# Performance work log

Measured on AMD Instinct MI355X. Metric: run time of the kernel, lower is better.

## Reference

```python
import jax, jax.numpy as jnp
import numpy as np

DIM = 16
FDIM = 16
KNN = 10
N = 1_000_000


def setup_inputs() -> dict:
    key = jax.random.key(0)
    k1, k2, k3, k4, k5, k6 = jax.random.split(key, 6)
    xknn = jax.random.normal(k1, (N, DIM, KNN), dtype=jnp.float32)
    x = jax.random.normal(k2, (N, DIM), dtype=jnp.float32)
    # mlpF = Conv1d(dim, F, 1): weight [F, dim] (kernel size 1 squeezed), bias [F]
    s = 1.0 / np.sqrt(DIM)
    Wf = jax.random.normal(k3, (FDIM, DIM), dtype=jnp.float32) * s
    bf = jax.random.normal(k4, (FDIM,), dtype=jnp.float32) * s
    # mlp1 = Conv1d(F, 1, 1): weight [F], bias scalar
    s1 = 1.0 / np.sqrt(FDIM)
    W1 = jax.random.normal(k5, (FDIM,), dtype=jnp.float32) * s1
    b1 = jax.random.normal(k6, (), dtype=jnp.float32) * s1
    return {"xknn": xknn, "x": x, "Wf": Wf, "bf": bf, "W1": W1, "b1": b1}


def reference(xknn, x, Wf, bf, W1, b1):
    n = xknn.shape[0]
    x2 = xknn.reshape(n, DIM, KNN)                       # [N, dim, K]
    # mlpF on neighbors: Conv1d(dim->F, k=1)
    h2 = jnp.einsum('fd,ndk->nfk', Wf, x2) + bf[:, None]  # [N, F, K]
    a2 = jnp.einsum('f,nfk->nk', W1, h2)[:, None, :] + b1  # mlp1 -> [N, 1, K]
    # mlpF + mlp1 on center point
    x1 = x.reshape(n, DIM, 1)
    h1 = jnp.einsum('fd,ndk->nfk', Wf, x1) + bf[:, None]   # [N, F, 1]
    a1 = jnp.einsum('f,nfk->nk', W1, h1) + b1              # [N, 1] (squeeze+unsqueeze)
    # per-slice additive attention logits (the python loop in the original)
    logits = a2 + a1[:, :, None]                           # [N, 1, K]
    # torch Fn.softmax with implicit dim on 3D tensor -> dim=0 (faithful)
    xc = jax.nn.softmax(logits, axis=0)                    # [N, 1, K]
    # values: mlpF(x2) again, then a raw reshape [N,F,K]->[N,K,F] (not transpose)
    x2v = h2.reshape(n, KNN, FDIM)                         # [N, K, F]
    x_attn = jnp.matmul(xc, x2v)                           # [N, 1, F]
    return x_attn.squeeze(), x2v
```

## Files before the change

### kernel.cpp

```cpp
#include <hip/hip_runtime.h>
#include <math.h>


__device__ __forceinline__ void comb(float& m, float& s, float om, float os) {
  float M = fmaxf(m, om);
  if (M == -INFINITY) return;
  s = s * __expf(m - M) + os * __expf(om - M);
  m = M;
}

template <int CTRL>
__device__ __forceinline__ float dppmov(float v) {
  return __int_as_float(__builtin_amdgcn_update_dpp(
      0, __float_as_int(v), CTRL, 0xf, 0xf, true));
}

__device__ __forceinline__ float osum(float v) {
  v += dppmov<0xB1>(v);
  v += dppmov<0x4E>(v);
  v += dppmov<0x141>(v);
  return v;
}

__device__ __forceinline__ float f4e(const float4& v, int e) {
  return (e == 0) ? v.x : (e == 1) ? v.y : (e == 2) ? v.z : v.w;
}

__global__ __launch_bounds__(256) void gap_k1(
    const float* __restrict__ xknn, const float* __restrict__ x,
    const float* __restrict__ Wf, const float* __restrict__ bf,
    const float* __restrict__ W1, const float* __restrict__ b1p,
    float* __restrict__ out, float* __restrict__ partials, int n) {
  __shared__ float s_red[4][16][2];

  const int tid = threadIdx.x;
  const int o = tid & 7;
  const int c = o & 3;
  const int p8 = tid >> 3;
  const int lane = tid & 63;
  const int wave = tid >> 6;

  float wfo[2][16], w1o[2], bfo[2];
#pragma unroll
  for (int fp = 0; fp < 2; ++fp) {
    const float* wr = Wf + (size_t)(2 * o + fp) * 16;
#pragma unroll
    for (int dq = 0; dq < 4; ++dq) {
      float4 v = *(const float4*)(wr + dq * 4);
      wfo[fp][dq * 4 + 0] = v.x;
      wfo[fp][dq * 4 + 1] = v.y;
      wfo[fp][dq * 4 + 2] = v.z;
      wfo[fp][dq * 4 + 3] = v.w;
    }
    w1o[fp] = W1[2 * o + fp];
    bfo[fp] = bf[2 * o + fp];
  }
  const float b1v = b1p[0];

  float u2[2];
  {
    float ufull[16];
#pragma unroll
    for (int d = 0; d < 16; ++d)
      ufull[d] = fmaf(w1o[1], wfo[1][d], w1o[0] * wfo[0][d]);
#pragma unroll
    for (int mk = 1; mk < 8; mk <<= 1)
#pragma unroll
      for (int d = 0; d < 16; ++d) ufull[d] += __shfl_xor(ufull[d], mk);
#pragma unroll
    for (int j = 0; j < 2; ++j) {
      float v = ufull[j];
#pragma unroll
      for (int oo = 1; oo < 8; ++oo) v = (o == oo) ? ufull[2 * oo + j] : v;
      u2[j] = v;
    }
  }
  float sb = fmaf(w1o[1], bfo[1], w1o[0] * bfo[0]);
  sb += __shfl_xor(sb, 1);
  sb += __shfl_xor(sb, 2);
  sb += __shfl_xor(sb, 4);
  const float addA = sb + 2.0f * b1v;

  float rm[2] = {-INFINITY, -INFINITY}, rs[2] = {0.f, 0.f};

  float* out0 = out;
  float* out1 = out + (size_t)n * 16;

  const long pt0 = (long)blockIdx.x * 32 + p8;
  const long pstride = (long)gridDim.x * 32;

  for (long pt = pt0; pt < n; pt += pstride) {
    const float* rowq = xknn + (size_t)pt * 160 + 40 * c;
    float4 own[10];
#pragma unroll
    for (int j = 0; j < 10; ++j) own[j] = *(const float4*)(rowq + 4 * j);
    const float2 xc = *(const float2*)(x + (size_t)pt * 16 + 2 * o);

    float acc0[10], acc1[10];
#pragma unroll
    for (int k = 0; k < 10; ++k) {
      acc0[k] = bfo[0];
      acc1[k] = bfo[1];
    }
#pragma unroll
    for (int src = 0; src < 4; ++src) {
#pragma unroll
      for (int rr = 0; rr < 40; ++rr) {
        const int r = 40 * src + rr;
        const int d = r / 10, k = r - d * 10;
        const float mine = f4e(own[rr >> 2], rr & 3);
        const float xv = (src == 0)   ? dppmov<0x00>(mine)
                         : (src == 1) ? dppmov<0x55>(mine)
                         : (src == 2) ? dppmov<0xAA>(mine)
                                      : dppmov<0xFF>(mine);
        acc0[k] = fmaf(wfo[0][d], xv, acc0[k]);
        acc1[k] = fmaf(wfo[1][d], xv, acc1[k]);
      }
    }

    float* o1 = out1 + (size_t)pt * 160 + 20 * o;
    *(float4*)(o1 + 0) = make_float4(acc0[0], acc0[1], acc0[2], acc0[3]);
    *(float4*)(o1 + 4) = make_float4(acc0[4], acc0[5], acc0[6], acc0[7]);
    *(float4*)(o1 + 8) = make_float4(acc0[8], acc0[9], acc1[0], acc1[1]);
    *(float4*)(o1 + 12) = make_float4(acc1[2], acc1[3], acc1[4], acc1[5]);
    *(float4*)(o1 + 16) = make_float4(acc1[6], acc1[7], acc1[8], acc1[9]);

    float tk[10];
#pragma unroll
    for (int k = 0; k < 10; ++k)
      tk[k] = osum(fmaf(w1o[1], acc1[k], w1o[0] * acc0[k]));

    const float a1u = osum(fmaf(u2[1], xc.y, u2[0] * xc.x));
    const float addc = a1u + addA;

    float lj0 = 0.f, lj1 = 0.f;
#pragma unroll
    for (int kk = 0; kk < 10; ++kk) {
      lj0 = (kk == 2 * o) ? (tk[kk] + addc) : lj0;
      lj1 = (kk == 2 * o + 1) ? (tk[kk] + addc) : lj1;
    }

    *(float2*)(out0 + (size_t)pt * 16 + 2 * o) = make_float2(lj0, lj1);
    if (o < 5) {
      comb(rm[0], rs[0], lj0, 1.0f);
      comb(rm[1], rs[1], lj1, 1.0f);
    }
  }

#pragma unroll
  for (int mk = 8; mk < 64; mk <<= 1) {
#pragma unroll
    for (int j = 0; j < 2; ++j) {
      float om = __shfl_xor(rm[j], mk);
      float os = __shfl_xor(rs[j], mk);
      comb(rm[j], rs[j], om, os);
    }
  }
  if (lane < 5) {
#pragma unroll
    for (int j = 0; j < 2; ++j) {
      s_red[wave][2 * lane + j][0] = rm[j];
      s_red[wave][2 * lane + j][1] = rs[j];
    }
  }
  __syncthreads();
  if (tid < 10) {
    float m = s_red[0][tid][0], s = s_red[0][tid][1];
    comb(m, s, s_red[1][tid][0], s_red[1][tid][1]);
    comb(m, s, s_red[2][tid][0], s_red[2][tid][1]);
    comb(m, s, s_red[3][tid][0], s_red[3][tid][1]);
    partials[(size_t)blockIdx.x * 20 + tid * 2 + 0] = m;
    partials[(size_t)blockIdx.x * 20 + tid * 2 + 1] = s;
  }
}

__global__ __launch_bounds__(256) void gap_k2(const float* __restrict__ part,
                                              int nb, float* __restrict__ fin) {
  const int k = blockIdx.x;
  const int tid = threadIdx.x;
  float m = -INFINITY, s = 0.f;
  for (int i = tid; i < nb; i += 256)
    comb(m, s, part[(size_t)i * 20 + k * 2], part[(size_t)i * 20 + k * 2 + 1]);
#pragma unroll
  for (int mask = 1; mask < 64; mask <<= 1) {
    float om = __shfl_xor(m, mask, 64);
    float os = __shfl_xor(s, mask, 64);
    comb(m, s, om, os);
  }
  __shared__ float sm[4][2];
  const int wave = tid >> 6, lane = tid & 63;
  if (lane == 0) { sm[wave][0] = m; sm[wave][1] = s; }
  __syncthreads();
  if (tid == 0) {
    for (int w = 1; w < 4; ++w) comb(m, s, sm[w][0], sm[w][1]);
    fin[k * 2 + 0] = m;
    fin[k * 2 + 1] = s;
  }
}

__global__ __launch_bounds__(256) void gap_k3(const float* __restrict__ fin,
                                              float* __restrict__ out, int n) {
  __shared__ float s_fin[20];
  if (threadIdx.x < 20) s_fin[threadIdx.x] = fin[threadIdx.x];
  __syncthreads();
  float mk[10], rsk[10];
#pragma unroll
  for (int k = 0; k < 10; ++k) {
    mk[k] = s_fin[2 * k];
    rsk[k] = 1.0f / s_fin[2 * k + 1];
  }
  float* out0 = out;
  const float* out1 = out + (size_t)n * 16;
  const int q = threadIdx.x & 3;
  const int pl = threadIdx.x >> 2;
  for (long i = (long)blockIdx.x * 64 + pl; i < n; i += (long)gridDim.x * 64) {
    float* lrow = out0 + i * 16;
    float4 la = *(const float4*)(lrow);
    float4 lb = *(const float4*)(lrow + 4);
    float2 lc = *(const float2*)(lrow + 8);
    float l[10] = {la.x, la.y, la.z, la.w, lb.x, lb.y, lb.z, lb.w, lc.x, lc.y};
    float w[10];
#pragma unroll
    for (int k = 0; k < 10; ++k) w[k] = __expf(l[k] - mk[k]) * rsk[k];
    const float* vrow = out1 + i * 160 + q * 4;
    float4 acc = make_float4(0.f, 0.f, 0.f, 0.f);
#pragma unroll
    for (int k = 0; k < 10; ++k) {
      float4 v = *(const float4*)(vrow + k * 16);
      float wk = w[k];
      acc.x = fmaf(wk, v.x, acc.x);
      acc.y = fmaf(wk, v.y, acc.y);
      acc.z = fmaf(wk, v.z, acc.z);
      acc.w = fmaf(wk, v.w, acc.w);
    }
    *(float4*)(lrow + q * 4) = acc;
  }
}

extern "C" void kernel_launch(void* const* d_in, const int* in_sizes, int n_in,
                              void* d_out, int out_size, void* d_ws, size_t ws_size,
                              hipStream_t stream) {
  const float* xknn = (const float*)d_in[0];
  const float* x    = (const float*)d_in[1];
  const float* Wf   = (const float*)d_in[2];
  const float* bf   = (const float*)d_in[3];
  const float* W1   = (const float*)d_in[4];
  const float* b1   = (const float*)d_in[5];
  float* out = (float*)d_out;
  const int n = in_sizes[1] / 16;

  const int G1 = 2048;
  float* partials = (float*)d_ws;
  float* finals = partials + (size_t)G1 * 20;

  gap_k1<<<G1, 256, 0, stream>>>(xknn, x, Wf, bf, W1, b1, out, partials, n);
  gap_k2<<<10, 256, 0, stream>>>(partials, G1, finals);
  gap_k3<<<2048, 256, 0, stream>>>(finals, out, n);
}
```

Measured before the change: 559.7 us.

## Remap gap_k1 to 16 lanes per point with one feature per lane

Restructures the main kernel so each point is handled by 16 lanes, each owning one output feature and ten contiguous inputs, instead of 8 lanes owning two features each. Cross-lane broadcast of inputs now uses ds_swizzle within 16-lane groups rather than DPP quad broadcasts. The W1·Wf vector is precomputed per lane directly, and launch_bounds is dropped. This halves per-thread register use and FMAs per point, but swizzles go through the LDS crossbar and may be slower than DPP. Memory accesses shrink to float2 granularity.

```diff
diff --git a/kernel.cpp b/kernel.cpp
--- a/kernel.cpp
+++ b/kernel.cpp
@@ -9,159 +9,134 @@
   m = M;
 }
 
+template <int B>
+__device__ __forceinline__ float swz16(float v) {
+  return __int_as_float(
+      __builtin_amdgcn_ds_swizzle(__float_as_int(v), (B << 5) | 0x10));
+}
+
 template <int CTRL>
 __device__ __forceinline__ float dppmov(float v) {
   return __int_as_float(__builtin_amdgcn_update_dpp(
       0, __float_as_int(v), CTRL, 0xf, 0xf, true));
 }
 
-__device__ __forceinline__ float osum(float v) {
+__device__ __forceinline__ float sum16(float v) {
   v += dppmov<0xB1>(v);
   v += dppmov<0x4E>(v);
   v += dppmov<0x141>(v);
+  v += dppmov<0x140>(v);
   return v;
 }
 
-__device__ __forceinline__ float f4e(const float4& v, int e) {
-  return (e == 0) ? v.x : (e == 1) ? v.y : (e == 2) ? v.z : v.w;
-}
-
-__global__ __launch_bounds__(256) void gap_k1(
+__global__ void gap_k1(
     const float* __restrict__ xknn, const float* __restrict__ x,
     const float* __restrict__ Wf, const float* __restrict__ bf,
     const float* __restrict__ W1, const float* __restrict__ b1p,
     float* __restrict__ out, float* __restrict__ partials, int n) {
-  __shared__ float s_red[4][16][2];
+  __shared__ float s_red[4][10][2];
 
   const int tid = threadIdx.x;
-  const int o = tid & 7;
-  const int c = o & 3;
-  const int p8 = tid >> 3;
   const int lane = tid & 63;
   const int wave = tid >> 6;
-
-  float wfo[2][16], w1o[2], bfo[2];
-#pragma unroll
-  for (int fp = 0; fp < 2; ++fp) {
-    const float* wr = Wf + (size_t)(2 * o + fp) * 16;
-#pragma unroll
-    for (int dq = 0; dq < 4; ++dq) {
-      float4 v = *(const float4*)(wr + dq * 4);
-      wfo[fp][dq * 4 + 0] = v.x;
-      wfo[fp][dq * 4 + 1] = v.y;
-      wfo[fp][dq * 4 + 2] = v.z;
-      wfo[fp][dq * 4 + 3] = v.w;
-    }
-    w1o[fp] = W1[2 * o + fp];
-    bfo[fp] = bf[2 * o + fp];
-  }
-  const float b1v = b1p[0];
-
-  float u2[2];
-  {
-    float ufull[16];
-#pragma unroll
-    for (int d = 0; d < 16; ++d)
-      ufull[d] = fmaf(w1o[1], wfo[1][d], w1o[0] * wfo[0][d]);
-#pragma unroll
-    for (int mk = 1; mk < 8; mk <<= 1)
-#pragma unroll
-      for (int d = 0; d < 16; ++d) ufull[d] += __shfl_xor(ufull[d], mk);
-#pragma unroll
-    for (int j = 0; j < 2; ++j) {
-      float v = ufull[j];
-#pragma unroll
-      for (int oo = 1; oo < 8; ++oo) v = (o == oo) ? ufull[2 * oo + j] : v;
-      u2[j] = v;
-    }
-  }
-  float sb = fmaf(w1o[1], bfo[1], w1o[0] * bfo[0]);
-  sb += __shfl_xor(sb, 1);
-  sb += __shfl_xor(sb, 2);
-  sb += __shfl_xor(sb, 4);
-  const float addA = sb + 2.0f * b1v;
-
-  float rm[2] = {-INFINITY, -INFINITY}, rs[2] = {0.f, 0.f};
+  const int f = lane & 15;
+  const int pg = lane >> 4;
+
+  float wfo[16];
+#pragma unroll
+  for (int dq = 0; dq < 4; ++dq) {
+    float4 v = *(const float4*)(Wf + (size_t)f * 16 + 4 * dq);
+    wfo[4 * dq + 0] = v.x;
+    wfo[4 * dq + 1] = v.y;
+    wfo[4 * dq + 2] = v.z;
+    wfo[4 * dq + 3] = v.w;
+  }
+  const float w1o = W1[f];
+  const float bfo = bf[f];
+  float u_own = 0.f;
+#pragma unroll
+  for (int j = 0; j < 16; ++j) u_own = fmaf(W1[j], Wf[j * 16 + f], u_own);
+  const float addA = 2.0f * b1p[0];
+
+  float rm = -INFINITY, rs = 0.f;
 
   float* out0 = out;
   float* out1 = out + (size_t)n * 16;
 
-  const long pt0 = (long)blockIdx.x * 32 + p8;
-  const long pstride = (long)gridDim.x * 32;
+  const long pt0 = (long)blockIdx.x * 16 + wave * 4 + pg;
+  const long pstride = (long)gridDim.x * 16;
 
   for (long pt = pt0; pt < n; pt += pstride) {
-    const float* rowq = xknn + (size_t)pt * 160 + 40 * c;
-    float4 own[10];
-#pragma unroll
-    for (int j = 0; j < 10; ++j) own[j] = *(const float4*)(rowq + 4 * j);
-    const float2 xc = *(const float2*)(x + (size_t)pt * 16 + 2 * o);
-
-    float acc0[10], acc1[10];
-#pragma unroll
-    for (int k = 0; k < 10; ++k) {
-      acc0[k] = bfo[0];
-      acc1[k] = bfo[1];
-    }
-#pragma unroll
-    for (int src = 0; src < 4; ++src) {
-#pragma unroll
-      for (int rr = 0; rr < 40; ++rr) {
-        const int r = 40 * src + rr;
-        const int d = r / 10, k = r - d * 10;
-        const float mine = f4e(own[rr >> 2], rr & 3);
-        const float xv = (src == 0)   ? dppmov<0x00>(mine)
-                         : (src == 1) ? dppmov<0x55>(mine)
-                         : (src == 2) ? dppmov<0xAA>(mine)
-                                      : dppmov<0xFF>(mine);
-        acc0[k] = fmaf(wfo[0][d], xv, acc0[k]);
-        acc1[k] = fmaf(wfo[1][d], xv, acc1[k]);
+    const float* rowf = xknn + (size_t)pt * 160 + 10 * f;
+    float2 own[5];
+#pragma unroll
+    for (int j = 0; j < 5; ++j) own[j] = *(const float2*)(rowf + 2 * j);
+    const float xo = x[(size_t)pt * 16 + f];
+
+    float acc[10];
+#pragma unroll
+    for (int k = 0; k < 10; ++k) acc[k] = bfo;
+#pragma unroll
+    for (int d = 0; d < 16; ++d) {
+#pragma unroll
+      for (int j = 0; j < 10; ++j) {
+        const float mine = (j & 1) ? own[j >> 1].y : own[j >> 1].x;
+        float xv;
+        switch (d) {
+          case 0:  xv = swz16<0>(mine); break;
+          case 1:  xv = swz16<1>(mine); break;
+          case 2:  xv = swz16<2>(mine); break;
+          case 3:  xv = swz16<3>(mine); break;
+          case 4:  xv = swz16<4>(mine); break;
+          case 5:  xv = swz16<5>(mine); break;
+          case 6:  xv = swz16<6>(mine); break;
+          case 7:  xv = swz16<7>(mine); break;
+          case 8:  xv = swz16<8>(mine); break;
+          case 9:  xv = swz16<9>(mine); break;
+          case 10: xv = swz16<10>(mine); break;
+          case 11: xv = swz16<11>(mine); break;
+          case 12: xv = swz16<12>(mine); break;
+          case 13: xv = swz16<13>(mine); break;
+          case 14: xv = swz16<14>(mine); break;
+          default: xv = swz16<15>(mine); break;
+        }
+        acc[j] = fmaf(wfo[d], xv, acc[j]);
       }
     }
 
-    float* o1 = out1 + (size_t)pt * 160 + 20 * o;
-    *(float4*)(o1 + 0) = make_float4(acc0[0], acc0[1], acc0[2], acc0[3]);
-    *(float4*)(o1 + 4) = make_float4(acc0[4], acc0[5], acc0[6], acc0[7]);
-    *(float4*)(o1 + 8) = make_float4(acc0[8], acc0[9], acc1[0], acc1[1]);
-    *(float4*)(o1 + 12) = make_float4(acc1[2], acc1[3], acc1[4], acc1[5]);
-    *(float4*)(o1 + 16) = make_float4(acc1[6], acc1[7], acc1[8], acc1[9]);
+    float* o1 = out1 + (size_t)pt * 160 + 10 * f;
+    *(float2*)(o1 + 0) = make_float2(acc[0], acc[1]);
+    *(float2*)(o1 + 2) = make_float2(acc[2], acc[3]);
+    *(float2*)(o1 + 4) = make_float2(acc[4], acc[5]);
+    *(float2*)(o1 + 6) = make_float2(acc[6], acc[7]);
+    *(float2*)(o1 + 8) = make_float2(acc[8], acc[9]);
 
     float tk[10];
 #pragma unroll
-    for (int k = 0; k < 10; ++k)
-      tk[k] = osum(fmaf(w1o[1], acc1[k], w1o[0] * acc0[k]));
-
-    const float a1u = osum(fmaf(u2[1], xc.y, u2[0] * xc.x));
+    for (int k = 0; k < 10; ++k) tk[k] = sum16(w1o * acc[k]);
+
+    const float a1u = sum16(u_own * xo);
     const float addc = a1u + addA;
 
-    float lj0 = 0.f, lj1 = 0.f;
-#pragma unroll
-    for (int kk = 0; kk < 10; ++kk) {
-      lj0 = (kk == 2 * o) ? (tk[kk] + addc) : lj0;
-      lj1 = (kk == 2 * o + 1) ? (tk[kk] + addc) : lj1;
+    float lj = 0.f;
+#pragma unroll
+    for (int kk = 0; kk < 10; ++kk) lj = (kk == f) ? (tk[kk] + addc) : lj;
+
+    if (f < 10) {
+      out0[(size_t)pt * 16 + f] = lj;
+      comb(rm, rs, lj, 1.0f);
     }
-
-    *(float2*)(out0 + (size_t)pt * 16 + 2 * o) = make_float2(lj0, lj1);
-    if (o < 5) {
-      comb(rm[0], rs[0], lj0, 1.0f);
-      comb(rm[1], rs[1], lj1, 1.0f);
-    }
-  }
-
-#pragma unroll
-  for (int mk = 8; mk < 64; mk <<= 1) {
-#pragma unroll
-    for (int j = 0; j < 2; ++j) {
-      float om = __shfl_xor(rm[j], mk);
-      float os = __shfl_xor(rs[j], mk);
-      comb(rm[j], rs[j], om, os);
-    }
-  }
-  if (lane < 5) {
-#pragma unroll
-    for (int j = 0; j < 2; ++j) {
-      s_red[wave][2 * lane + j][0] = rm[j];
-      s_red[wave][2 * lane + j][1] = rs[j];
-    }
+  }
+
+  {
+    float om = __shfl_xor(rm, 16), os = __shfl_xor(rs, 16);
+    comb(rm, rs, om, os);
+    om = __shfl_xor(rm, 32); os = __shfl_xor(rs, 32);
+    comb(rm, rs, om, os);
+  }
+  if (lane < 10) {
+    s_red[wave][lane][0] = rm;
+    s_red[wave][lane][1] = rs;
   }
   __syncthreads();
   if (tid < 10) {
```

After: 1.308 ms. 2.34x slower.
